# Kernel optimization log

Measured on AMD Instinct MI355X. Metric: run time of the kernel, lower is better.

Reference implementation:

```python
import jax, jax.numpy as jnp
import numpy as np

B, N, IN_DIM, DIM, KNN = 8, 2048, 128, 128, 16
POS_H = 64
ATTN_H = DIM * 4
EPS = 1e-5
SCALE = 1.0 / np.sqrt(DIM).astype(np.float32)


def setup_inputs() -> dict:
    key = jax.random.key(0)
    ks = jax.random.split(key, 10)
    nrm = lambda k, shape, s=0.02: jax.random.normal(k, shape, jnp.float32) * s
    return dict(
        ori_x=jax.random.normal(ks[0], (B, N, IN_DIM), jnp.float32),
        pos=jax.random.normal(ks[1], (B, N, 3), jnp.float32),
        w_in=nrm(ks[2], (IN_DIM, DIM)),
        w_qkv=nrm(ks[3], (DIM, 3 * DIM)),
        w_out=nrm(ks[4], (DIM, IN_DIM)),
        pos_w1=nrm(ks[5], (3, POS_H)), pos_b1=jnp.zeros((POS_H,), jnp.float32),
        pos_bn_g=jnp.ones((POS_H,), jnp.float32), pos_bn_b=jnp.zeros((POS_H,), jnp.float32),
        pos_bn_m=jnp.zeros((POS_H,), jnp.float32), pos_bn_v=jnp.ones((POS_H,), jnp.float32),
        pos_w2=nrm(ks[6], (POS_H, DIM)), pos_b2=jnp.zeros((DIM,), jnp.float32),
        attn_w1=nrm(ks[7], (DIM, ATTN_H)), attn_b1=jnp.zeros((ATTN_H,), jnp.float32),
        attn_bn_g=jnp.ones((ATTN_H,), jnp.float32), attn_bn_b=jnp.zeros((ATTN_H,), jnp.float32),
        attn_bn_m=jnp.zeros((ATTN_H,), jnp.float32), attn_bn_v=jnp.ones((ATTN_H,), jnp.float32),
        attn_w2=nrm(ks[8], (ATTN_H, DIM)), attn_b2=jnp.zeros((DIM,), jnp.float32),
    )


def _bn_eval(x, g, b, m, v):
    # BatchNorm2d in eval mode; channel is the last axis in our [b,n,k,C] layout
    return (x - m) * (g * jax.lax.rsqrt(v + EPS)) + b


def reference(ori_x, pos, w_in, w_qkv, w_out,
              pos_w1, pos_b1, pos_bn_g, pos_bn_b, pos_bn_m, pos_bn_v, pos_w2, pos_b2,
              attn_w1, attn_b1, attn_bn_g, attn_bn_b, attn_bn_m, attn_bn_v, attn_w2, attn_b2):
    x = ori_x @ w_in                                  # [b,n,dim]
    qkv = x @ w_qkv
    q, k, v = jnp.split(qkv, 3, axis=-1)              # each [b,n,dim]

    # pairwise squared distances [b,n,n] (monotone in rel_dist -> same topk)
    sq = jnp.sum(pos * pos, axis=-1)
    d2 = sq[:, :, None] + sq[:, None, :] - 2.0 * jnp.einsum('bnd,bmd->bnm', pos, pos)
    _, idx = jax.lax.top_k(-d2, KNN)                  # [b,n,KNN] nearest neighbors

    gather = jax.vmap(lambda t, i: t[i])              # [n,C],[n,k] -> [n,k,C] per batch
    k_g = gather(k, idx)                              # [b,n,k,dim]
    v_g = gather(v, idx)
    pos_g = gather(pos, idx)                          # [b,n,k,3]

    rel_pos = pos[:, :, None, :] - pos_g              # [b,n,k,3]
    pe = jax.nn.relu(_bn_eval(rel_pos @ pos_w1 + pos_b1, pos_bn_g, pos_bn_b, pos_bn_m, pos_bn_v))
    pe = pe @ pos_w2 + pos_b2                         # [b,n,k,dim]

    qk_rel = q[:, :, None, :] - k_g                   # [b,n,k,dim]
    h = jax.nn.relu(_bn_eval((qk_rel + pe) @ attn_w1 + attn_b1,
                             attn_bn_g, attn_bn_b, attn_bn_m, attn_bn_v))
    h = h @ attn_w2 + attn_b2                         # [b,n,k,dim]

    attn = jax.nn.softmax(h * SCALE, axis=-2)         # softmax over neighbors
    agg = jnp.sum(attn * (v_g + pe), axis=2)          # [b,n,dim]
    return agg @ w_out + ori_x
```

## Files before the change

kernel.cpp:

```cpp
#include <hip/hip_runtime.h>

#define EPS 1e-5f

constexpr int NB   = 8;
constexpr int NN   = 2048;
constexpr int DIM  = 128;
constexpr int KNN  = 16;
constexpr int AH   = 512;
constexpr int NPTS = NB * NN;
constexpr float SCALE = 0.08838834764831845f;

typedef __attribute__((ext_vector_type(8))) short short8;
typedef __attribute__((ext_vector_type(4))) float floatx4;

__device__ __forceinline__ short f2bf(float f) {
  union { float f; unsigned u; } a; a.f = f;
  return (short)((a.u + 0x8000u) >> 16);
}
__device__ __forceinline__ float bf2f(short s) {
  union { unsigned u; float f; } a; a.u = ((unsigned)(unsigned short)s) << 16;
  return a.f;
}

__global__ __launch_bounds__(256) void pack_weights(
    const float* __restrict__ attn_w1, const float* __restrict__ attn_w2,
    const float* __restrict__ pos_w2, const float* __restrict__ w_in,
    const float* __restrict__ w_qkv,
    const float* __restrict__ w_out, const float* __restrict__ pos,
    const float* __restrict__ attn_b1, const float* __restrict__ abn_g,
    const float* __restrict__ abn_b, const float* __restrict__ abn_m,
    const float* __restrict__ abn_v,
    const float* __restrict__ pos_b1, const float* __restrict__ pbn_g,
    const float* __restrict__ pbn_b, const float* __restrict__ pbn_m,
    const float* __restrict__ pbn_v, const float* __restrict__ pos_b2,
    short* __restrict__ w1p, short* __restrict__ w2p, short* __restrict__ pw2p,
    short* __restrict__ wfp, short* __restrict__ wop,
    float* __restrict__ biasq,
    float* __restrict__ t1sc, float* __restrict__ t1bi,
    float* __restrict__ phsc, float* __restrict__ phbi,
    float* __restrict__ pos_t)
{
  int t = blockIdx.x * 256 + threadIdx.x;
  if (t < 65536) {
    int j = t & 7, lane = (t >> 3) & 63, ks = (t >> 9) & 3, nt = (t >> 11) & 3, ch = t >> 13;
    int q = lane >> 4, cc = lane & 15;
    int k = ks * 32 + q * 8 + j, n = ch * 64 + nt * 16 + cc;
    w1p[t] = f2bf(attn_w1[(size_t)k * AH + n]);
  } else if (t < 131072) {
    int e = t - 65536;
    int j = e & 7, lane = (e >> 3) & 63, ks = (e >> 9) & 1, nt = (e >> 10) & 7, ch = e >> 13;
    int q = lane >> 4, cc = lane & 15;
    int k = ch * 64 + ks * 32 + q * 8 + j, n = nt * 16 + cc;
    w2p[e] = f2bf(attn_w2[(size_t)k * DIM + n]);
  } else if (t < 139264) {
    int e = t - 131072;
    int j = e & 7, lane = (e >> 3) & 63, ks = (e >> 9) & 1, nt = e >> 10;
    int q = lane >> 4, cc = lane & 15;
    int k = ks * 32 + q * 8 + j, n = nt * 16 + cc;
    pw2p[e] = f2bf(pos_w2[(size_t)k * DIM + n]);
  } else if (t < 188416) {
    int e = t - 139264;
    int j = e & 7, lane = (e >> 3) & 63, ks = (e >> 9) & 3, nt = (e >> 11) & 7, nc = e >> 14;
    int q = lane >> 4, cc = lane & 15;
    int k = ks * 32 + q * 8 + j, n = nc * 128 + nt * 16 + cc;
    float s = 0.0f;
#pragma unroll 8
    for (int m = 0; m < 128; ++m)
      s += w_in[(size_t)k * DIM + m] * w_qkv[(size_t)m * 384 + n];
    wfp[e] = f2bf(s);
  } else if (t < 204800) {
    int e = t - 188416;
    int j = e & 7, lane = (e >> 3) & 63, ks = (e >> 9) & 3, nt = (e >> 11) & 7;
    int q = lane >> 4, cc = lane & 15;
    int k = ks * 32 + q * 8 + j, n = nt * 16 + cc;
    wop[e] = f2bf(w_out[(size_t)k * DIM + n]);
  } else if (t < 205184) {
    int c = t - 204800;
    biasq[c] = (c < 128) ? pos_b2[c] : ((c < 256) ? 0.0f : pos_b2[c - 256]);
  } else if (t < 205696) {
    int c = t - 205184;
    t1sc[c] = abn_g[c] * rsqrtf(abn_v[c] + EPS);
  } else if (t < 206208) {
    int c = t - 205696;
    float sc = abn_g[c] * rsqrtf(abn_v[c] + EPS);
    t1bi[c] = (attn_b1[c] - abn_m[c]) * sc + abn_b[c];
  } else if (t < 206272) {
    int c = t - 206208;
    phsc[c] = pbn_g[c] * rsqrtf(pbn_v[c] + EPS);
  } else if (t < 206336) {
    int c = t - 206272;
    float sc = pbn_g[c] * rsqrtf(pbn_v[c] + EPS);
    phbi[c] = (pos_b1[c] - pbn_m[c]) * sc + pbn_b[c];
  } else if (t < 206336 + NPTS * 3) {
    int e = t - 206336;
    int p = e / 3, d = e - p * 3;
    int b = p >> 11, n = p & (NN - 1);
    pos_t[((size_t)b * 3 + d) * NN + n] = pos[e];
  }
}

__global__ __launch_bounds__(256, 4) void gemm_in(
    const float* __restrict__ A, const short* __restrict__ wfp,
    const float* __restrict__ biasq, short* __restrict__ C)
{
  __shared__ short As[64 * 128];
  const int tid = threadIdx.x;
  const int lane = tid & 63, w = tid >> 6;
  const int wr = w >> 1, wc = w & 1;
  const int q = lane >> 4, cc = lane & 15;
  const int row0 = blockIdx.x * 64;
#pragma unroll
  for (int it = 0; it < 4; ++it) {
    int e = tid + it * 256;
    int row = e >> 4, cg = e & 15;
    const float* src = A + (size_t)(row0 + row) * 128 + cg * 8;
    float4 f0 = *(const float4*)src, f1 = *(const float4*)(src + 4);
    short8 v;
    v[0] = f2bf(f0.x); v[1] = f2bf(f0.y); v[2] = f2bf(f0.z); v[3] = f2bf(f0.w);
    v[4] = f2bf(f1.x); v[5] = f2bf(f1.y); v[6] = f2bf(f1.z); v[7] = f2bf(f1.w);
    *(short8*)(As + row * 128 + ((cg ^ (row & 15)) << 3)) = v;
  }
  __syncthreads();
  for (int nc = 0; nc < 3; ++nc) {
    floatx4 acc[2][4];
#pragma unroll
    for (int i = 0; i < 2; ++i)
#pragma unroll
      for (int jt = 0; jt < 4; ++jt) acc[i][jt] = (floatx4){0.f, 0.f, 0.f, 0.f};
#pragma unroll
    for (int ks = 0; ks < 4; ++ks) {
      short8 a8[2], b8[4];
#pragma unroll
      for (int i = 0; i < 2; ++i) {
        int row = (wr * 2 + i) * 16 + cc;
        a8[i] = *(const short8*)(As + row * 128 + (((ks * 4 + q) ^ cc) << 3));
      }
#pragma unroll
      for (int jt = 0; jt < 4; ++jt)
        b8[jt] = *(const short8*)(wfp + ((((nc * 8 + wc * 4 + jt) * 4 + ks) * 64 + lane) << 3));
#pragma unroll
      for (int i = 0; i < 2; ++i)
#pragma unroll
        for (int jt = 0; jt < 4; ++jt)
          acc[i][jt] = __builtin_amdgcn_mfma_f32_16x16x32_bf16(a8[i], b8[jt], acc[i][jt], 0, 0, 0);
    }
#pragma unroll
    for (int jt = 0; jt < 4; ++jt) {
      int colG = nc * 128 + (wc * 4 + jt) * 16 + cc;
      float bv = biasq[colG];
#pragma unroll
      for (int i = 0; i < 2; ++i)
#pragma unroll
        for (int r = 0; r < 4; ++r) {
          int row = (wr * 2 + i) * 16 + q * 4 + r;
          C[(size_t)(row0 + row) * 384 + colG] = f2bf(acc[i][jt][r] + bv);
        }
    }
  }
}

__global__ __launch_bounds__(256, 3) void fused_attn(
    const float* __restrict__ pos_t, const short* __restrict__ qkv,
    const float* __restrict__ pos_w1,
    const short* __restrict__ w1p, const short* __restrict__ w2p,
    const short* __restrict__ pw2p, const short* __restrict__ wop,
    const float* __restrict__ t1sc, const float* __restrict__ t1bi,
    const float* __restrict__ phsc, const float* __restrict__ phbi,
    const float* __restrict__ attn_b2,
    const float* __restrict__ ori_x, float* __restrict__ out)
{
  __shared__ short a_s[64 * 128];
  __shared__ short vpe_s[64 * 128];
  __shared__ short t1_s[2][64 * 64];
  __shared__ short q_ss[4 * 128];
  __shared__ float relp_s[64 * 4];
  __shared__ int   nbr_s[64];

  const int tid = threadIdx.x;
  const int lane = tid & 63, w = tid >> 6;
  const int wr = w >> 1, wc = w & 1;
  const int q = lane >> 4, cc = lane & 15;
  const int bb = blockIdx.x & 7;
  const int base = (blockIdx.x >> 3) * 4;
  const int gp0 = bb * NN + base;

  const float* px = pos_t + (size_t)bb * 3 * NN;
  const float* py = px + NN;
  const float* pz = py + NN;

  {
    const int il = base + w;
    const float xi = px[il], yi = py[il], zi = pz[il];
    const float sqi = xi * xi + yi * yi + zi * zi;
    float v[32];
#pragma unroll
    for (int t = 0; t < 32; ++t) {
      int j = t * 64 + lane;
      float xj = px[j], yj = py[j], zj = pz[j];
      float sqj = xj * xj + yj * yj + zj * zj;
      float dot = xi * xj + yi * yj + zi * zj;
      v[t] = sqi + sqj - 2.0f * dot;
    }
    for (int s = 0; s < KNN; ++s) {
      float bv = 3.4e38f; int bj = 1 << 30;
#pragma unroll
      for (int t = 0; t < 32; ++t) {
        if (v[t] < bv) { bv = v[t]; bj = t * 64 + lane; }
      }
#pragma unroll
      for (int m = 1; m < 64; m <<= 1) {
        float ov = __shfl_xor(bv, m);
        int   oj = __shfl_xor(bj, m);
        if (ov < bv || (ov == bv && oj < bj)) { bv = ov; bj = oj; }
      }
      if (lane == 0) nbr_s[w * KNN + s] = bj;
#pragma unroll
      for (int t = 0; t < 32; ++t)
        if (bj == t * 64 + lane) v[t] = 3.4e38f;
    }
  }
  __syncthreads();

  if (tid < 64) {
    int p = tid >> 4;
    int j = nbr_s[tid];
    relp_s[tid * 4 + 0] = px[base + p] - px[j];
    relp_s[tid * 4 + 1] = py[base + p] - py[j];
    relp_s[tid * 4 + 2] = pz[base + p] - pz[j];
  } else if (tid < 128) {
    int e = tid - 64;
    int p = e >> 4, seg = e & 15;
    *(short8*)(q_ss + p * 128 + seg * 8) =
        *(const short8*)(qkv + (size_t)(gp0 + p) * 384 + seg * 8);
  }
  __syncthreads();

#pragma unroll
  for (int r2 = 0; r2 < 16; ++r2) {
    int e = tid + r2 * 256;
    int row = e >> 6, c = e & 63;
    float lin = relp_s[row * 4] * pos_w1[c] + relp_s[row * 4 + 1] * pos_w1[64 + c]
              + relp_s[row * 4 + 2] * pos_w1[128 + c];
    t1_s[0][row * 64 + (((c >> 3) ^ (row & 7)) << 3) + (c & 7)] =
        f2bf(fmaxf(lin * phsc[c] + phbi[c], 0.0f));
  }
  __syncthreads();

  floatx4 pe[2][4];
#pragma unroll
  for (int i = 0; i < 2; ++i)
#pragma unroll
    for (int jt = 0; jt < 4; ++jt) pe[i][jt] = (floatx4){0.f, 0.f, 0.f, 0.f};
#pragma unroll
  for (int ks = 0; ks < 2; ++ks) {
    short8 a8[2];
#pragma unroll
    for (int i = 0; i < 2; ++i) {
      int row = (wr * 2 + i) * 16 + cc;
      a8[i] = *(const short8*)(t1_s[0] + row * 64 + (((ks * 4 + q) ^ (row & 7)) << 3));
    }
#pragma unroll
    for (int jt = 0; jt < 4; ++jt) {
      short8 b8 = *(const short8*)(pw2p + ((((wc * 4 + jt) * 2 + ks) * 64 + lane) << 3));
#pragma unroll
      for (int i = 0; i < 2; ++i)
        pe[i][jt] = __builtin_amdgcn_mfma_f32_16x16x32_bf16(a8[i], b8, pe[i][jt], 0, 0, 0);
    }
  }

#pragma unroll
  for (int i = 0; i < 2; ++i) {
    int rt = wr * 2 + i;
#pragma unroll
    for (int jt = 0; jt < 4; ++jt) {
      int col = (wc * 4 + jt) * 16 + cc;
      float qv = bf2f(q_ss[rt * 128 + col]);
#pragma unroll
      for (int r = 0; r < 4; ++r) {
        int row = rt * 16 + q * 4 + r;
        const short* kv = qkv + ((size_t)bb * NN + nbr_s[row]) * 384;
        float pev = pe[i][jt][r];
        int slot = row * 128 + (((col >> 3) ^ (row & 15)) << 3) + (col & 7);
        a_s[slot]   = f2bf(qv - bf2f(kv[128 + col]) + pev);
        vpe_s[slot] = f2bf(bf2f(kv[256 + col]) + pev);
      }
    }
  }
  __syncthreads();

  floatx4 hacc[2][4];
#pragma unroll
  for (int i = 0; i < 2; ++i)
#pragma unroll
    for (int jt = 0; jt < 4; ++jt) hacc[i][jt] = (floatx4){0.f, 0.f, 0.f, 0.f};

  for (int ch = 0; ch < 8; ++ch) {
    short* t1b = t1_s[ch & 1];
    floatx4 tacc[2][2];
#pragma unroll
    for (int i = 0; i < 2; ++i)
#pragma unroll
      for (int jt = 0; jt < 2; ++jt) tacc[i][jt] = (floatx4){0.f, 0.f, 0.f, 0.f};
#pragma unroll
    for (int ks = 0; ks < 4; ++ks) {
      short8 a8[2], b8[2];
#pragma unroll
      for (int i = 0; i < 2; ++i) {
        int row = (wr * 2 + i) * 16 + cc;
        a8[i] = *(const short8*)(a_s + row * 128 + (((ks * 4 + q) ^ cc) << 3));
      }
#pragma unroll
      for (int jt = 0; jt < 2; ++jt)
        b8[jt] = *(const short8*)(w1p + ((((ch * 4 + wc * 2 + jt) * 4 + ks) * 64 + lane) << 3));
#pragma unroll
      for (int i = 0; i < 2; ++i)
#pragma unroll
        for (int jt = 0; jt < 2; ++jt)
          tacc[i][jt] = __builtin_amdgcn_mfma_f32_16x16x32_bf16(a8[i], b8[jt], tacc[i][jt], 0, 0, 0);
    }
#pragma unroll
    for (int jt = 0; jt < 2; ++jt) {
      int colL = (wc * 2 + jt) * 16 + cc;
      int colG = ch * 64 + colL;
      float sc = t1sc[colG], bi = t1bi[colG];
#pragma unroll
      for (int i = 0; i < 2; ++i)
#pragma unroll
        for (int r = 0; r < 4; ++r) {
          int row = (wr * 2 + i) * 16 + q * 4 + r;
          t1b[row * 64 + (((colL >> 3) ^ (row & 7)) << 3) + (colL & 7)] =
              f2bf(fmaxf(tacc[i][jt][r] * sc + bi, 0.0f));
        }
    }
    __syncthreads();
#pragma unroll
    for (int ks = 0; ks < 2; ++ks) {
      short8 a8[2], b8[4];
#pragma unroll
      for (int i = 0; i < 2; ++i) {
        int row = (wr * 2 + i) * 16 + cc;
        a8[i] = *(const short8*)(t1b + row * 64 + (((ks * 4 + q) ^ (row & 7)) << 3));
      }
#pragma unroll
      for (int jt = 0; jt < 4; ++jt)
        b8[jt] = *(const short8*)(w2p + ((((ch * 8 + wc * 4 + jt) * 2 + ks) * 64 + lane) << 3));
#pragma unroll
      for (int i = 0; i < 2; ++i)
#pragma unroll
        for (int jt = 0; jt < 4; ++jt)
          hacc[i][jt] = __builtin_amdgcn_mfma_f32_16x16x32_bf16(a8[i], b8[jt], hacc[i][jt], 0, 0, 0);
    }
  }

  short* agg_s = t1_s[0];
#pragma unroll
  for (int r2 = 0; r2 < 6; ++r2) {
    int e = tid + r2 * 256;
    agg_s[(4 + (e >> 7)) * 128 + (e & 127)] = 0;
  }
#pragma unroll
  for (int i = 0; i < 2; ++i) {
    int rt = wr * 2 + i;
#pragma unroll
    for (int jt = 0; jt < 4; ++jt) {
      int col = (wc * 4 + jt) * 16 + cc;
      float b2v = attn_b2[col];
      float v0[4], mx = -3.4e38f;
#pragma unroll
      for (int r = 0; r < 4; ++r) {
        v0[r] = (hacc[i][jt][r] + b2v) * SCALE;
        mx = fmaxf(mx, v0[r]);
      }
      mx = fmaxf(mx, __shfl_xor(mx, 16));
      mx = fmaxf(mx, __shfl_xor(mx, 32));
      float ex[4], sum = 0.f;
#pragma unroll
      for (int r = 0; r < 4; ++r) { ex[r] = __expf(v0[r] - mx); sum += ex[r]; }
      sum += __shfl_xor(sum, 16);
      sum += __shfl_xor(sum, 32);
      float inv = 1.0f / sum;
      float part = 0.f;
#pragma unroll
      for (int r = 0; r < 4; ++r) {
        int row = rt * 16 + q * 4 + r;
        int slot = row * 128 + (((col >> 3) ^ (row & 15)) << 3) + (col & 7);
        part += ex[r] * bf2f(vpe_s[slot]);
      }
      part += __shfl_xor(part, 16);
      part += __shfl_xor(part, 32);
      if (q == 0) agg_s[rt * 128 + col] = f2bf(part * inv);
    }
  }
  __syncthreads();

  {
    floatx4 oacc[2];
#pragma unroll
    for (int jt = 0; jt < 2; ++jt) oacc[jt] = (floatx4){0.f, 0.f, 0.f, 0.f};
#pragma unroll
    for (int ks = 0; ks < 4; ++ks) {
      short8 a8 = *(const short8*)(agg_s + cc * 128 + ks * 32 + q * 8);
#pragma unroll
      for (int jt = 0; jt < 2; ++jt) {
        short8 b8 = *(const short8*)(wop + ((((w * 2 + jt) * 4 + ks) * 64 + lane) << 3));
        oacc[jt] = __builtin_amdgcn_mfma_f32_16x16x32_bf16(a8, b8, oacc[jt], 0, 0, 0);
      }
    }
    if (q == 0) {
#pragma unroll
      for (int jt = 0; jt < 2; ++jt) {
        int col = (w * 2 + jt) * 16 + cc;
#pragma unroll
        for (int r = 0; r < 4; ++r) {
          size_t o = (size_t)(gp0 + r) * 128 + col;
          out[o] = oacc[jt][r] + ori_x[o];
        }
      }
    }
  }
}

extern "C" void kernel_launch(void* const* d_in, const int* in_sizes, int n_in,
                              void* d_out, int out_size, void* d_ws, size_t ws_size,
                              hipStream_t stream)
{
  const float* ori_x    = (const float*)d_in[0];
  const float* pos      = (const float*)d_in[1];
  const float* w_in     = (const float*)d_in[2];
  const float* w_qkv    = (const float*)d_in[3];
  const float* w_out    = (const float*)d_in[4];
  const float* pos_w1   = (const float*)d_in[5];
  const float* pos_b1   = (const float*)d_in[6];
  const float* pos_bn_g = (const float*)d_in[7];
  const float* pos_bn_b = (const float*)d_in[8];
  const float* pos_bn_m = (const float*)d_in[9];
  const float* pos_bn_v = (const float*)d_in[10];
  const float* pos_w2   = (const float*)d_in[11];
  const float* pos_b2   = (const float*)d_in[12];
  const float* attn_w1  = (const float*)d_in[13];
  const float* attn_b1  = (const float*)d_in[14];
  const float* attn_bn_g = (const float*)d_in[15];
  const float* attn_bn_b = (const float*)d_in[16];
  const float* attn_bn_m = (const float*)d_in[17];
  const float* attn_bn_v = (const float*)d_in[18];
  const float* attn_w2  = (const float*)d_in[19];
  const float* attn_b2  = (const float*)d_in[20];
  float* out = (float*)d_out;

  short* qkvb = (short*)d_ws;
  short* w1p  = qkvb + (size_t)NPTS * 3 * DIM;
  short* w2p  = w1p + 65536;
  short* pw2p = w2p + 65536;
  short* wfp  = pw2p + 8192;
  short* wop  = wfp + 49152;
  float* biasq = (float*)(wop + 16384);
  float* t1sc = biasq + 384;
  float* t1bi = t1sc + 512;
  float* phsc = t1bi + 512;
  float* phbi = phsc + 64;
  float* pos_t = phbi + 64;

  pack_weights<<<998, 256, 0, stream>>>(attn_w1, attn_w2, pos_w2, w_in, w_qkv,
      w_out, pos,
      attn_b1, attn_bn_g, attn_bn_b, attn_bn_m, attn_bn_v,
      pos_b1, pos_bn_g, pos_bn_b, pos_bn_m, pos_bn_v, pos_b2,
      w1p, w2p, pw2p, wfp, wop, biasq, t1sc, t1bi, phsc, phbi, pos_t);
  gemm_in<<<NPTS / 64, 256, 0, stream>>>(ori_x, wfp, biasq, qkvb);
  fused_attn<<<NPTS / 4, 256, 0, stream>>>(pos_t, qkvb, pos_w1,
      w1p, w2p, pw2p, wop, t1sc, t1bi, phsc, phbi, attn_b2, ori_x, out);
}
```

Before: 369.8 us.

## Move KNN search out of attention kernel into merged KNN+QKV GEMM launch

The brute-force KNN top-16 selection leaves the fused attention kernel and now runs inside the input GEMM kernel. Blocks are interleaved so every 17th does a GEMM tile and the others do KNN for 4 points each, writing neighbour indices to a workspace buffer. The attention kernel then just loads the indices. This lightens the heavily register-bound attention kernel and lets the KNN work run at higher occupancy next to the GEMM, at the cost of an extra global index round trip. The merged kernel's register use is now set by the KNN branch.

```diff
diff --git a/kernel.cpp b/kernel.cpp
--- a/kernel.cpp
+++ b/kernel.cpp
@@ -99,68 +99,110 @@
   }
 }
 
-__global__ __launch_bounds__(256, 4) void gemm_in(
+__global__ __launch_bounds__(256, 4) void knn_gemm_in(
     const float* __restrict__ A, const short* __restrict__ wfp,
-    const float* __restrict__ biasq, short* __restrict__ C)
+    const float* __restrict__ biasq, short* __restrict__ C,
+    const float* __restrict__ pos_t, int* __restrict__ idx_out)
 {
   __shared__ short As[64 * 128];
   const int tid = threadIdx.x;
-  const int lane = tid & 63, w = tid >> 6;
-  const int wr = w >> 1, wc = w & 1;
-  const int q = lane >> 4, cc = lane & 15;
-  const int row0 = blockIdx.x * 64;
-#pragma unroll
-  for (int it = 0; it < 4; ++it) {
-    int e = tid + it * 256;
-    int row = e >> 4, cg = e & 15;
-    const float* src = A + (size_t)(row0 + row) * 128 + cg * 8;
-    float4 f0 = *(const float4*)src, f1 = *(const float4*)(src + 4);
-    short8 v;
-    v[0] = f2bf(f0.x); v[1] = f2bf(f0.y); v[2] = f2bf(f0.z); v[3] = f2bf(f0.w);
-    v[4] = f2bf(f1.x); v[5] = f2bf(f1.y); v[6] = f2bf(f1.z); v[7] = f2bf(f1.w);
-    *(short8*)(As + row * 128 + ((cg ^ (row & 15)) << 3)) = v;
-  }
-  __syncthreads();
-  for (int nc = 0; nc < 3; ++nc) {
-    floatx4 acc[2][4];
-#pragma unroll
-    for (int i = 0; i < 2; ++i)
-#pragma unroll
-      for (int jt = 0; jt < 4; ++jt) acc[i][jt] = (floatx4){0.f, 0.f, 0.f, 0.f};
-#pragma unroll
-    for (int ks = 0; ks < 4; ++ks) {
-      short8 a8[2], b8[4];
-#pragma unroll
-      for (int i = 0; i < 2; ++i) {
-        int row = (wr * 2 + i) * 16 + cc;
-        a8[i] = *(const short8*)(As + row * 128 + (((ks * 4 + q) ^ cc) << 3));
-      }
-#pragma unroll
-      for (int jt = 0; jt < 4; ++jt)
-        b8[jt] = *(const short8*)(wfp + ((((nc * 8 + wc * 4 + jt) * 4 + ks) * 64 + lane) << 3));
+  const int bx = blockIdx.x;
+
+  if (bx % 17 == 0) {
+    const int lane = tid & 63, w = tid >> 6;
+    const int wr = w >> 1, wc = w & 1;
+    const int q = lane >> 4, cc = lane & 15;
+    const int row0 = (bx / 17) * 64;
+#pragma unroll
+    for (int it = 0; it < 4; ++it) {
+      int e = tid + it * 256;
+      int row = e >> 4, cg = e & 15;
+      const float* src = A + (size_t)(row0 + row) * 128 + cg * 8;
+      float4 f0 = *(const float4*)src, f1 = *(const float4*)(src + 4);
+      short8 v;
+      v[0] = f2bf(f0.x); v[1] = f2bf(f0.y); v[2] = f2bf(f0.z); v[3] = f2bf(f0.w);
+      v[4] = f2bf(f1.x); v[5] = f2bf(f1.y); v[6] = f2bf(f1.z); v[7] = f2bf(f1.w);
+      *(short8*)(As + row * 128 + ((cg ^ (row & 15)) << 3)) = v;
+    }
+    __syncthreads();
+    for (int nc = 0; nc < 3; ++nc) {
+      floatx4 acc[2][4];
 #pragma unroll
       for (int i = 0; i < 2; ++i)
 #pragma unroll
+        for (int jt = 0; jt < 4; ++jt) acc[i][jt] = (floatx4){0.f, 0.f, 0.f, 0.f};
+#pragma unroll
+      for (int ks = 0; ks < 4; ++ks) {
+        short8 a8[2], b8[4];
+#pragma unroll
+        for (int i = 0; i < 2; ++i) {
+          int row = (wr * 2 + i) * 16 + cc;
+          a8[i] = *(const short8*)(As + row * 128 + (((ks * 4 + q) ^ cc) << 3));
+        }
+#pragma unroll
         for (int jt = 0; jt < 4; ++jt)
-          acc[i][jt] = __builtin_amdgcn_mfma_f32_16x16x32_bf16(a8[i], b8[jt], acc[i][jt], 0, 0, 0);
-    }
-#pragma unroll
-    for (int jt = 0; jt < 4; ++jt) {
-      int colG = nc * 128 + (wc * 4 + jt) * 16 + cc;
-      float bv = biasq[colG];
-#pragma unroll
-      for (int i = 0; i < 2; ++i)
-#pragma unroll
-        for (int r = 0; r < 4; ++r) {
-          int row = (wr * 2 + i) * 16 + q * 4 + r;
-          C[(size_t)(row0 + row) * 384 + colG] = f2bf(acc[i][jt][r] + bv);
-        }
+          b8[jt] = *(const short8*)(wfp + ((((nc * 8 + wc * 4 + jt) * 4 + ks) * 64 + lane) << 3));
+#pragma unroll
+        for (int i = 0; i < 2; ++i)
+#pragma unroll
+          for (int jt = 0; jt < 4; ++jt)
+            acc[i][jt] = __builtin_amdgcn_mfma_f32_16x16x32_bf16(a8[i], b8[jt], acc[i][jt], 0, 0, 0);
+      }
+#pragma unroll
+      for (int jt = 0; jt < 4; ++jt) {
+        int colG = nc * 128 + (wc * 4 + jt) * 16 + cc;
+        float bv = biasq[colG];
+#pragma unroll
+        for (int i = 0; i < 2; ++i)
+#pragma unroll
+          for (int r = 0; r < 4; ++r) {
+            int row = (wr * 2 + i) * 16 + q * 4 + r;
+            C[(size_t)(row0 + row) * 384 + colG] = f2bf(acc[i][jt][r] + bv);
+          }
+      }
+    }
+  } else {
+    const int kb = bx - bx / 17 - 1;
+    const int lane = tid & 63;
+    const int p = kb * 4 + (tid >> 6);
+    const int b = p >> 11, i = p & (NN - 1);
+    const float* px = pos_t + (size_t)b * 3 * NN;
+    const float* py = px + NN;
+    const float* pz = py + NN;
+    const float xi = px[i], yi = py[i], zi = pz[i];
+    const float sqi = xi * xi + yi * yi + zi * zi;
+    float v[32];
+#pragma unroll
+    for (int t = 0; t < 32; ++t) {
+      int j = t * 64 + lane;
+      float xj = px[j], yj = py[j], zj = pz[j];
+      float sqj = xj * xj + yj * yj + zj * zj;
+      float dot = xi * xj + yi * yj + zi * zj;
+      v[t] = sqi + sqj - 2.0f * dot;
+    }
+    for (int s = 0; s < KNN; ++s) {
+      float bv = 3.4e38f; int bj = 1 << 30;
+#pragma unroll
+      for (int t = 0; t < 32; ++t) {
+        if (v[t] < bv) { bv = v[t]; bj = t * 64 + lane; }
+      }
+#pragma unroll
+      for (int m = 1; m < 64; m <<= 1) {
+        float ov = __shfl_xor(bv, m);
+        int   oj = __shfl_xor(bj, m);
+        if (ov < bv || (ov == bv && oj < bj)) { bv = ov; bj = oj; }
+      }
+      if (lane == 0) idx_out[(size_t)p * KNN + s] = bj;
+#pragma unroll
+      for (int t = 0; t < 32; ++t)
+        if (bj == t * 64 + lane) v[t] = 3.4e38f;
     }
   }
 }
 
 __global__ __launch_bounds__(256, 3) void fused_attn(
     const float* __restrict__ pos_t, const short* __restrict__ qkv,
+    const int* __restrict__ knn_idx,
     const float* __restrict__ pos_w1,
     const short* __restrict__ w1p, const short* __restrict__ w2p,
     const short* __restrict__ pw2p, const short* __restrict__ wop,
@@ -188,50 +230,20 @@
   const float* py = px + NN;
   const float* pz = py + NN;
 
-  {
-    const int il = base + w;
-    const float xi = px[il], yi = py[il], zi = pz[il];
-    const float sqi = xi * xi + yi * yi + zi * zi;
-    float v[32];
-#pragma unroll
-    for (int t = 0; t < 32; ++t) {
-      int j = t * 64 + lane;
-      float xj = px[j], yj = py[j], zj = pz[j];
-      float sqj = xj * xj + yj * yj + zj * zj;
-      float dot = xi * xj + yi * yj + zi * zj;
-      v[t] = sqi + sqj - 2.0f * dot;
-    }
-    for (int s = 0; s < KNN; ++s) {
-      float bv = 3.4e38f; int bj = 1 << 30;
-#pragma unroll
-      for (int t = 0; t < 32; ++t) {
-        if (v[t] < bv) { bv = v[t]; bj = t * 64 + lane; }
-      }
-#pragma unroll
-      for (int m = 1; m < 64; m <<= 1) {
-        float ov = __shfl_xor(bv, m);
-        int   oj = __shfl_xor(bj, m);
-        if (ov < bv || (ov == bv && oj < bj)) { bv = ov; bj = oj; }
-      }
-      if (lane == 0) nbr_s[w * KNN + s] = bj;
-#pragma unroll
-      for (int t = 0; t < 32; ++t)
-        if (bj == t * 64 + lane) v[t] = 3.4e38f;
-    }
+  if (tid < 64) nbr_s[tid] = knn_idx[(size_t)gp0 * KNN + tid];
+  else if (tid < 128) {
+    int e = tid - 64;
+    int p = e >> 4, seg = e & 15;
+    *(short8*)(q_ss + p * 128 + seg * 8) =
+        *(const short8*)(qkv + (size_t)(gp0 + p) * 384 + seg * 8);
   }
   __syncthreads();
-
   if (tid < 64) {
     int p = tid >> 4;
     int j = nbr_s[tid];
     relp_s[tid * 4 + 0] = px[base + p] - px[j];
     relp_s[tid * 4 + 1] = py[base + p] - py[j];
     relp_s[tid * 4 + 2] = pz[base + p] - pz[j];
-  } else if (tid < 128) {
-    int e = tid - 64;
-    int p = e >> 4, seg = e & 15;
-    *(short8*)(q_ss + p * 128 + seg * 8) =
-        *(const short8*)(qkv + (size_t)(gp0 + p) * 384 + seg * 8);
   }
   __syncthreads();
 
@@ -459,13 +471,14 @@
   float* phsc = t1bi + 512;
   float* phbi = phsc + 64;
   float* pos_t = phbi + 64;
+  int*   idx  = (int*)(pos_t + (size_t)NB * 3 * NN);
 
   pack_weights<<<998, 256, 0, stream>>>(attn_w1, attn_w2, pos_w2, w_in, w_qkv,
       w_out, pos,
       attn_b1, attn_bn_g, attn_bn_b, attn_bn_m, attn_bn_v,
       pos_b1, pos_bn_g, pos_bn_b, pos_bn_m, pos_bn_v, pos_b2,
       w1p, w2p, pw2p, wfp, wop, biasq, t1sc, t1bi, phsc, phbi, pos_t);
-  gemm_in<<<NPTS / 64, 256, 0, stream>>>(ori_x, wfp, biasq, qkvb);
-  fused_attn<<<NPTS / 4, 256, 0, stream>>>(pos_t, qkvb, pos_w1,
+  knn_gemm_in<<<4352, 256, 0, stream>>>(ori_x, wfp, biasq, qkvb, pos_t, idx);
+  fused_attn<<<NPTS / 4, 256, 0, stream>>>(pos_t, qkvb, idx, pos_w1,
       w1p, w2p, pw2p, wop, t1sc, t1bi, phsc, phbi, attn_b2, ori_x, out);
 }
```

Result: no change. 366.1 us (-1.0%).
